# Kernel optimization log

Measured on AMD Instinct MI355X. Metric: run time of the kernel, lower is better.

Reference implementation:

```python
import jax, jax.numpy as jnp
import numpy as np

NUM_ENT = 7
DIM_ENT = 4
NEMBED_HALF = 128  # nembed_ctx / 2
BATCH = 16384


def setup_inputs() -> dict:
    key = jax.random.key(0)
    k1, k2, k3, k4, k5 = jax.random.split(key, 5)
    ctx = jax.random.normal(k1, (NUM_ENT * DIM_ENT, BATCH), dtype=jnp.float32)
    init = 0.01
    w_prop = jax.random.uniform(k2, (DIM_ENT, NEMBED_HALF), jnp.float32, -init, init)
    b_prop = jax.random.uniform(k3, (NEMBED_HALF,), jnp.float32, -init, init)
    w_rel = jax.random.uniform(k4, (DIM_ENT + 1, NEMBED_HALF), jnp.float32, -init, init)
    b_rel = jax.random.uniform(k5, (NEMBED_HALF,), jnp.float32, -init, init)
    return {"ctx": ctx, "w_prop": w_prop, "b_prop": b_prop, "w_rel": w_rel, "b_rel": b_rel}


def reference(ctx, w_prop, b_prop, w_rel, b_rel):
    # ctx: [num_ent*dim_ent, B] -> ents: [B, num_ent, dim_ent]
    ents = ctx.T.reshape(-1, NUM_ENT, DIM_ENT)
    # property embedding: Linear + ReLU (dropout = identity at inference)
    prop_emb = jax.nn.relu(jnp.einsum('bnd,dh->bnh', ents, w_prop) + b_prop)
    # pairwise diffs [B, i, j, d] and euclidean distance over first two coords
    diffs = ents[:, :, None, :] - ents[:, None, :, :]
    dist = jnp.sqrt(diffs[..., 0] ** 2 + diffs[..., 1] ** 2)  # [B, i, j]
    feats = jnp.concatenate([diffs, dist[..., None]], axis=-1)  # [B, i, j, dim_ent+1]
    rel = jax.nn.relu(jnp.einsum('bijd,dh->bijh', feats, w_rel) + b_rel)
    # original loops skip i == j: zero the diagonal before summing over j
    off_diag = (1.0 - jnp.eye(NUM_ENT, dtype=rel.dtype))[None, :, :, None]
    rel_emb = jnp.sum(rel * off_diag, axis=2)  # [B, num_ent, H]
    return jnp.concatenate([prop_emb, rel_emb], axis=2)  # [B, num_ent, 2H]
```

## Files before the change

kernel.cpp:

```cpp
#include <hip/hip_runtime.h>

#define NUM_ENT 7
#define DIM_ENT 4
#define H 128
#define OUTC (2 * H)
#define BPB 8

__global__ __launch_bounds__(256) void ace_kernel(
    const float* __restrict__ ctx,
    const float* __restrict__ w_prop,
    const float* __restrict__ b_prop,
    const float* __restrict__ w_rel,
    const float* __restrict__ b_rel,
    float* __restrict__ out,
    int B)
{
    __shared__ float s_ents[BPB][NUM_ENT * DIM_ENT];
    __shared__ float s_feat[BPB][NUM_ENT][NUM_ENT][5];

    const int tid = threadIdx.x;
    const int b0 = blockIdx.x * BPB;

    if (tid < BPB * NUM_ENT * DIM_ENT) {
        const int k  = tid >> 3;
        const int bb = tid & 7;
        s_ents[bb][k] = ctx[(size_t)k * B + (b0 + bb)];
    }
    __syncthreads();

    for (int t = tid; t < BPB * NUM_ENT * NUM_ENT; t += 256) {
        const int bb = t / (NUM_ENT * NUM_ENT);
        const int p  = t % (NUM_ENT * NUM_ENT);
        const int i  = p / NUM_ENT;
        const int j  = p % NUM_ENT;
        const float dx = s_ents[bb][i * 4 + 0] - s_ents[bb][j * 4 + 0];
        const float dy = s_ents[bb][i * 4 + 1] - s_ents[bb][j * 4 + 1];
        const float dz = s_ents[bb][i * 4 + 2] - s_ents[bb][j * 4 + 2];
        const float dw = s_ents[bb][i * 4 + 3] - s_ents[bb][j * 4 + 3];
        s_feat[bb][i][j][0] = dx;
        s_feat[bb][i][j][1] = dy;
        s_feat[bb][i][j][2] = dz;
        s_feat[bb][i][j][3] = dw;
        s_feat[bb][i][j][4] = sqrtf(dx * dx + dy * dy);
    }
    __syncthreads();

    const int w    = tid >> 6;
    const int lane = tid & 63;
    const int bb   = w * 2 + (lane >> 5);
    const int c4   = (lane & 31) << 2;
    float* outb = out + (size_t)(b0 + bb) * (NUM_ENT * OUTC);

    {
        const float4 w0 = *(const float4*)(w_rel + 0 * H + c4);
        const float4 w1 = *(const float4*)(w_rel + 1 * H + c4);
        const float4 w2 = *(const float4*)(w_rel + 2 * H + c4);
        const float4 w3 = *(const float4*)(w_rel + 3 * H + c4);
        const float4 w4 = *(const float4*)(w_rel + 4 * H + c4);
        const float4 br = *(const float4*)(b_rel + c4);
#pragma unroll
        for (int i = 0; i < NUM_ENT; ++i) {
            float4 acc = {0.f, 0.f, 0.f, 0.f};
#pragma unroll
            for (int j = 0; j < NUM_ENT; ++j) {
                if (j == i) continue;
                const float f0 = s_feat[bb][i][j][0];
                const float f1 = s_feat[bb][i][j][1];
                const float f2 = s_feat[bb][i][j][2];
                const float f3 = s_feat[bb][i][j][3];
                const float f4 = s_feat[bb][i][j][4];
                acc.x += fmaxf(br.x + f0 * w0.x + f1 * w1.x + f2 * w2.x + f3 * w3.x + f4 * w4.x, 0.f);
                acc.y += fmaxf(br.y + f0 * w0.y + f1 * w1.y + f2 * w2.y + f3 * w3.y + f4 * w4.y, 0.f);
                acc.z += fmaxf(br.z + f0 * w0.z + f1 * w1.z + f2 * w2.z + f3 * w3.z + f4 * w4.z, 0.f);
                acc.w += fmaxf(br.w + f0 * w0.w + f1 * w1.w + f2 * w2.w + f3 * w3.w + f4 * w4.w, 0.f);
            }
            *(float4*)(outb + i * OUTC + H + c4) = acc;
        }
    }

    {
        const float4 w0 = *(const float4*)(w_prop + 0 * H + c4);
        const float4 w1 = *(const float4*)(w_prop + 1 * H + c4);
        const float4 w2 = *(const float4*)(w_prop + 2 * H + c4);
        const float4 w3 = *(const float4*)(w_prop + 3 * H + c4);
        const float4 bp = *(const float4*)(b_prop + c4);
#pragma unroll
        for (int n = 0; n < NUM_ENT; ++n) {
            const float e0 = s_ents[bb][n * 4 + 0];
            const float e1 = s_ents[bb][n * 4 + 1];
            const float e2 = s_ents[bb][n * 4 + 2];
            const float e3 = s_ents[bb][n * 4 + 3];
            float4 a;
            a.x = fmaxf(bp.x + e0 * w0.x + e1 * w1.x + e2 * w2.x + e3 * w3.x, 0.f);
            a.y = fmaxf(bp.y + e0 * w0.y + e1 * w1.y + e2 * w2.y + e3 * w3.y, 0.f);
            a.z = fmaxf(bp.z + e0 * w0.z + e1 * w1.z + e2 * w2.z + e3 * w3.z, 0.f);
            a.w = fmaxf(bp.w + e0 * w0.w + e1 * w1.w + e2 * w2.w + e3 * w3.w, 0.f);
            *(float4*)(outb + n * OUTC + c4) = a;
        }
    }
}

extern "C" void kernel_launch(void* const* d_in, const int* in_sizes, int n_in,
                              void* d_out, int out_size, void* d_ws, size_t ws_size,
                              hipStream_t stream) {
    const float* ctx    = (const float*)d_in[0];
    const float* w_prop = (const float*)d_in[1];
    const float* b_prop = (const float*)d_in[2];
    const float* w_rel  = (const float*)d_in[3];
    const float* b_rel  = (const float*)d_in[4];
    float* out = (float*)d_out;

    const int B = in_sizes[0] / (NUM_ENT * DIM_ENT);
    const int nb = (B + BPB - 1) / BPB;
    ace_kernel<<<nb, 256, 0, stream>>>(ctx, w_prop, b_prop, w_rel, b_rel, out, B);
}
```

Baseline: 132.6 us.

## Compute pairwise features in registers, drop shared feature staging, use nontemporal stores

Removes the shared-memory pairwise feature table and its extra barrier. Each thread now loads its seven entities into registers and recomputes the diffs and distance inline, using the hardware sqrt builtin. Output writes become nontemporal stores, and the prop and rel sections are swapped in order. This trades redundant per-thread ALU work for fewer LDS accesses and one less sync, and the fast sqrt may differ slightly in precision.

```diff
diff --git a/kernel.cpp b/kernel.cpp
--- a/kernel.cpp
+++ b/kernel.cpp
@@ -5,6 +5,8 @@
 #define H 128
 #define OUTC (2 * H)
 #define BPB 8
+
+typedef float f32x4 __attribute__((ext_vector_type(4)));
 
 __global__ __launch_bounds__(256) void ace_kernel(
     const float* __restrict__ ctx,
@@ -16,7 +18,6 @@
     int B)
 {
     __shared__ float s_ents[BPB][NUM_ENT * DIM_ENT];
-    __shared__ float s_feat[BPB][NUM_ENT][NUM_ENT][5];
 
     const int tid = threadIdx.x;
     const int b0 = blockIdx.x * BPB;
@@ -28,74 +29,59 @@
     }
     __syncthreads();
 
-    for (int t = tid; t < BPB * NUM_ENT * NUM_ENT; t += 256) {
-        const int bb = t / (NUM_ENT * NUM_ENT);
-        const int p  = t % (NUM_ENT * NUM_ENT);
-        const int i  = p / NUM_ENT;
-        const int j  = p % NUM_ENT;
-        const float dx = s_ents[bb][i * 4 + 0] - s_ents[bb][j * 4 + 0];
-        const float dy = s_ents[bb][i * 4 + 1] - s_ents[bb][j * 4 + 1];
-        const float dz = s_ents[bb][i * 4 + 2] - s_ents[bb][j * 4 + 2];
-        const float dw = s_ents[bb][i * 4 + 3] - s_ents[bb][j * 4 + 3];
-        s_feat[bb][i][j][0] = dx;
-        s_feat[bb][i][j][1] = dy;
-        s_feat[bb][i][j][2] = dz;
-        s_feat[bb][i][j][3] = dw;
-        s_feat[bb][i][j][4] = sqrtf(dx * dx + dy * dy);
-    }
-    __syncthreads();
-
     const int w    = tid >> 6;
     const int lane = tid & 63;
     const int bb   = w * 2 + (lane >> 5);
     const int c4   = (lane & 31) << 2;
     float* outb = out + (size_t)(b0 + bb) * (NUM_ENT * OUTC);
 
+    f32x4 e[NUM_ENT];
+#pragma unroll
+    for (int n = 0; n < NUM_ENT; ++n)
+        e[n] = *(const f32x4*)(&s_ents[bb][n * DIM_ENT]);
+
     {
-        const float4 w0 = *(const float4*)(w_rel + 0 * H + c4);
-        const float4 w1 = *(const float4*)(w_rel + 1 * H + c4);
-        const float4 w2 = *(const float4*)(w_rel + 2 * H + c4);
-        const float4 w3 = *(const float4*)(w_rel + 3 * H + c4);
-        const float4 w4 = *(const float4*)(w_rel + 4 * H + c4);
-        const float4 br = *(const float4*)(b_rel + c4);
+        const f32x4 w0 = *(const f32x4*)(w_prop + 0 * H + c4);
+        const f32x4 w1 = *(const f32x4*)(w_prop + 1 * H + c4);
+        const f32x4 w2 = *(const f32x4*)(w_prop + 2 * H + c4);
+        const f32x4 w3 = *(const f32x4*)(w_prop + 3 * H + c4);
+        const f32x4 bp = *(const f32x4*)(b_prop + c4);
 #pragma unroll
-        for (int i = 0; i < NUM_ENT; ++i) {
-            float4 acc = {0.f, 0.f, 0.f, 0.f};
-#pragma unroll
-            for (int j = 0; j < NUM_ENT; ++j) {
-                if (j == i) continue;
-                const float f0 = s_feat[bb][i][j][0];
-                const float f1 = s_feat[bb][i][j][1];
-                const float f2 = s_feat[bb][i][j][2];
-                const float f3 = s_feat[bb][i][j][3];
-                const float f4 = s_feat[bb][i][j][4];
-                acc.x += fmaxf(br.x + f0 * w0.x + f1 * w1.x + f2 * w2.x + f3 * w3.x + f4 * w4.x, 0.f);
-                acc.y += fmaxf(br.y + f0 * w0.y + f1 * w1.y + f2 * w2.y + f3 * w3.y + f4 * w4.y, 0.f);
-                acc.z += fmaxf(br.z + f0 * w0.z + f1 * w1.z + f2 * w2.z + f3 * w3.z + f4 * w4.z, 0.f);
-                acc.w += fmaxf(br.w + f0 * w0.w + f1 * w1.w + f2 * w2.w + f3 * w3.w + f4 * w4.w, 0.f);
-            }
-            *(float4*)(outb + i * OUTC + H + c4) = acc;
+        for (int n = 0; n < NUM_ENT; ++n) {
+            const float e0 = e[n].x, e1 = e[n].y, e2 = e[n].z, e3 = e[n].w;
+            f32x4 a;
+            a.x = fmaxf(bp.x + e0 * w0.x + e1 * w1.x + e2 * w2.x + e3 * w3.x, 0.f);
+            a.y = fmaxf(bp.y + e0 * w0.y + e1 * w1.y + e2 * w2.y + e3 * w3.y, 0.f);
+            a.z = fmaxf(bp.z + e0 * w0.z + e1 * w1.z + e2 * w2.z + e3 * w3.z, 0.f);
+            a.w = fmaxf(bp.w + e0 * w0.w + e1 * w1.w + e2 * w2.w + e3 * w3.w, 0.f);
+            __builtin_nontemporal_store(a, (f32x4*)(outb + n * OUTC + c4));
         }
     }
 
     {
-        const float4 w0 = *(const float4*)(w_prop + 0 * H + c4);
-        const float4 w1 = *(const float4*)(w_prop + 1 * H + c4);
-        const float4 w2 = *(const float4*)(w_prop + 2 * H + c4);
-        const float4 w3 = *(const float4*)(w_prop + 3 * H + c4);
-        const float4 bp = *(const float4*)(b_prop + c4);
+        const f32x4 w0 = *(const f32x4*)(w_rel + 0 * H + c4);
+        const f32x4 w1 = *(const f32x4*)(w_rel + 1 * H + c4);
+        const f32x4 w2 = *(const f32x4*)(w_rel + 2 * H + c4);
+        const f32x4 w3 = *(const f32x4*)(w_rel + 3 * H + c4);
+        const f32x4 w4 = *(const f32x4*)(w_rel + 4 * H + c4);
+        const f32x4 br = *(const f32x4*)(b_rel + c4);
 #pragma unroll
-        for (int n = 0; n < NUM_ENT; ++n) {
-            const float e0 = s_ents[bb][n * 4 + 0];
-            const float e1 = s_ents[bb][n * 4 + 1];
-            const float e2 = s_ents[bb][n * 4 + 2];
-            const float e3 = s_ents[bb][n * 4 + 3];
-            float4 a;
-            a.x = fmaxf(bp.x + e0 * w0.x + e1 * w1.x + e2 * w2.x + e3 * w3.x, 0.f);
-            a.y = fmaxf(bp.y + e0 * w0.y + e1 * w1.y + e2 * w2.y + e3 * w3.y, 0.f);
-            a.z = fmaxf(bp.z + e0 * w0.z + e1 * w1.z + e2 * w2.z + e3 * w3.z, 0.f);
-            a.w = fmaxf(bp.w + e0 * w0.w + e1 * w1.w + e2 * w2.w + e3 * w3.w, 0.f);
-            *(float4*)(outb + n * OUTC + c4) = a;
+        for (int i = 0; i < NUM_ENT; ++i) {
+            f32x4 acc = {0.f, 0.f, 0.f, 0.f};
+#pragma unroll
+            for (int j = 0; j < NUM_ENT; ++j) {
+                if (j == i) continue;
+                const float dx = e[i].x - e[j].x;
+                const float dy = e[i].y - e[j].y;
+                const float dz = e[i].z - e[j].z;
+                const float dv = e[i].w - e[j].w;
+                const float d  = __builtin_amdgcn_sqrtf(dx * dx + dy * dy);
+                acc.x += fmaxf(br.x + dx * w0.x + dy * w1.x + dz * w2.x + dv * w3.x + d * w4.x, 0.f);
+                acc.y += fmaxf(br.y + dx * w0.y + dy * w1.y + dz * w2.y + dv * w3.y + d * w4.y, 0.f);
+                acc.z += fmaxf(br.z + dx * w0.z + dy * w1.z + dz * w2.z + dv * w3.z + d * w4.z, 0.f);
+                acc.w += fmaxf(br.w + dx * w0.w + dy * w1.w + dz * w2.w + dv * w3.w + d * w4.w, 0.f);
+            }
+            __builtin_nontemporal_store(acc, (f32x4*)(outb + i * OUTC + H + c4));
         }
     }
 }
```

New measurement: 140.9 us. +6.2%, slower.
